# Performance work log

Measured on AMD Instinct MI355X. Metric: run time of the kernel, lower is better.

## Reference

```python
import jax, jax.numpy as jnp
import numpy as np

LAT = 512
FIN = 256
FOUT = 256
K = 3
N_STYLE = 4
B, H, W = 16, 64, 64


def setup_inputs() -> dict:
    key = jax.random.key(0)
    ks = jax.random.split(key, 8)
    x = jax.random.normal(ks[0], (B, FIN, H, W), dtype=jnp.float32)
    lat = jax.random.normal(ks[1], (B, LAT), dtype=jnp.float32)
    # main conv weight, kaiming_normal fan_in, leaky_relu a=0 -> gain sqrt(2)
    fan_in = FIN * K * K
    weight = jax.random.normal(ks[2], (FOUT, FIN, K, K), dtype=jnp.float32) * np.float32(np.sqrt(2.0 / fan_in))
    # EqualLinear layers: raw weight ~ N(0,1), runtime-scaled by 1/sqrt(in_dim)
    ws = jax.random.normal(ks[3], (N_STYLE, LAT, LAT), dtype=jnp.float32)
    bs = jnp.zeros((N_STYLE, LAT), dtype=jnp.float32)
    # final plain nn.Linear(lat_size, fin): uniform(-1/sqrt(in), 1/sqrt(in))
    bound = np.float32(1.0 / np.sqrt(LAT))
    wf = jax.random.uniform(ks[4], (FIN, LAT), dtype=jnp.float32, minval=-bound, maxval=bound)
    bf = jax.random.uniform(ks[5], (FIN,), dtype=jnp.float32, minval=-bound, maxval=bound)
    return {"x": x, "lat": lat, "weight": weight, "ws": ws, "bs": bs, "wf": wf, "bf": bf}


def reference(x, lat, weight, ws, bs, wf, bf):
    Bb, fin, Hh, Ww = x.shape
    fout, _, k, _ = weight.shape
    eq_scale = np.float32(1.0 / np.sqrt(lat.shape[1]))  # EqualLinear runtime scale

    # style MLP: n_layers_style x (EqualLinear + LeakyReLU(0.2)), then Linear -> fin
    h = lat
    for i in range(ws.shape[0]):
        h = jax.nn.leaky_relu(h @ (ws[i] * eq_scale).T + bs[i], 0.2)
    styles = h @ wf.T + bf  # [B, fin]

    # normalize base weight by inf-norm over (fin,k,k) per output channel
    wnorm = jnp.max(jnp.abs(weight), axis=(1, 2, 3), keepdims=True)
    mw = weight * (np.float32(1.0 / np.sqrt(fin * k * k)) / wnorm)  # [fout,fin,k,k]
    # normalize styles by inf-norm per sample
    styles = styles / jnp.max(jnp.abs(styles), axis=1, keepdims=True)

    # per-sample modulation + demodulation
    w = mw[None] * styles[:, None, :, None, None]  # [B,fout,fin,k,k]
    dcoefs = jax.lax.rsqrt(jnp.sum(w * w, axis=(2, 3, 4)) + 1e-8)  # [B,fout]
    w = w * dcoefs[:, :, None, None, None]
    w = w.reshape(Bb * fout, fin, k, k)

    # grouped conv with groups = batch (stride/dilation NOT passed in original -> 1)
    pad = (k - 1) // 2  # _get_same_padding with stride=1, dilation=1
    xg = x.reshape(1, Bb * fin, Hh, Ww)
    y = jax.lax.conv_general_dilated(
        xg, w, window_strides=(1, 1), padding=[(pad, pad), (pad, pad)],
        dimension_numbers=("NCHW", "OIHW", "NCHW"), feature_group_count=Bb)
    return y.reshape(Bb, fout, Hh, Ww)
```

## Files before the change

kernel.cpp:

```cpp
#include <hip/hip_runtime.h>
#include <hip/hip_bf16.h>

#define LATN 512
#define FINN 256
#define FOUTN 256
#define NB 16
#define HH 64
#define WW 64

typedef __attribute__((ext_vector_type(8))) short bf16x8;
typedef __attribute__((ext_vector_type(4))) float f32x4;
typedef __attribute__((ext_vector_type(4))) int i32x4;

#define WS_ZERO   0
#define WS_MW2    4096
#define WS_DCO    266240
#define WS_SNORM  282624
#define WS_WFMT   299008
#define WS_XM     1478656
#define WS_HA     (WS_XM)
#define WS_HB     (WS_XM + 32768)
#define WS_STY    (WS_XM + 65536)

__global__ void weight_prep_kernel(const float* __restrict__ weight,
                                   __hip_bfloat16* __restrict__ wfmt,
                                   float* __restrict__ mw2sum,
                                   float* __restrict__ zerobuf) {
    __shared__ float red[256];
    int o = blockIdx.x, t = threadIdx.x;
    if (o == 0 && t < 64) zerobuf[t] = 0.f;
    const float* wrow = weight + ((size_t)o * FINN + t) * 9;
    float wv[9];
    float mx = 0.f;
    #pragma unroll
    for (int k = 0; k < 9; ++k) { wv[k] = wrow[k]; mx = fmaxf(mx, fabsf(wv[k])); }
    red[t] = mx;
    __syncthreads();
    for (int k = 128; k > 0; k >>= 1) {
        if (t < k) red[t] = fmaxf(red[t], red[t + k]);
        __syncthreads();
    }
    float scale = (1.0f / 48.0f) / red[0];
    int obi = o >> 6, ol = o & 63, ch = t >> 5, il = t & 31;
    int slot = (il >> 3) ^ ((ol >> 1) & 3);
    char* basep = (char*)wfmt + (size_t)obi * 294912 + (size_t)ch * 36864
                + (size_t)ol * 64 + slot * 16 + (il & 7) * 2;
    float s2 = 0.f;
    #pragma unroll
    for (int tap = 0; tap < 9; ++tap) {
        float m = wv[tap] * scale;
        s2 += m * m;
        *(__hip_bfloat16*)(basep + tap * 4096) = __float2bfloat16(m);
    }
    mw2sum[(size_t)o * FINN + t] = s2;
}

__global__ __launch_bounds__(256) void style_layer_kernel(
    const float* __restrict__ in, const float* __restrict__ w,
    const float* __restrict__ bias, float* __restrict__ out,
    int in_dim_v4, int out_dim, float scale, int do_lrelu) {
    int t = threadIdx.x;
    int jl = t >> 4, kl = t & 15;
    int j = blockIdx.x * 16 + jl;
    int b = blockIdx.y;
    const float4* inr = (const float4*)(in + (size_t)b * (in_dim_v4 * 4));
    const float4* wr  = (const float4*)(w + (size_t)j * (in_dim_v4 * 4));
    float sum = 0.f;
    #pragma unroll 4
    for (int kb = kl; kb < in_dim_v4; kb += 16) {
        float4 wv = wr[kb], iv = inr[kb];
        sum += wv.x * iv.x + wv.y * iv.y + wv.z * iv.z + wv.w * iv.w;
    }
    #pragma unroll
    for (int off = 8; off >= 1; off >>= 1)
        sum += __shfl_xor(sum, off, 16);
    if (kl == 0) {
        float v = sum * scale + bias[j];
        if (do_lrelu && v < 0.f) v *= 0.2f;
        out[(size_t)b * out_dim + j] = v;
    }
}

__global__ __launch_bounds__(256) void norm_dcoef_kernel(
    const float* __restrict__ sty, const float* __restrict__ mw2,
    float* __restrict__ snorm, float* __restrict__ dco) {
    __shared__ float red[256];
    __shared__ float s2[256];
    int b = blockIdx.x, t = threadIdx.x;
    float v = sty[(size_t)b * FINN + t];
    red[t] = fabsf(v);
    __syncthreads();
    for (int k = 128; k > 0; k >>= 1) {
        if (t < k) red[t] = fmaxf(red[t], red[t + k]);
        __syncthreads();
    }
    float sv = v / red[0];
    snorm[(size_t)b * FINN + t] = sv;
    s2[t] = sv * sv;
    __syncthreads();
    const float4* m2 = (const float4*)(mw2 + (size_t)t * FINN);
    const float4* sq = (const float4*)s2;
    float sum = 0.f;
    #pragma unroll 8
    for (int kb = 0; kb < 64; ++kb) {
        float4 a = m2[kb], xq = sq[kb];
        sum += a.x * xq.x + a.y * xq.y + a.z * xq.z + a.w * xq.w;
    }
    dco[(size_t)b * FOUTN + t] = rsqrtf(sum + 1e-8f);
}

__global__ __launch_bounds__(256) void xcvt_kernel(const float* __restrict__ x,
                                                   const float* __restrict__ sn,
                                                   char* __restrict__ xm) {
    __shared__ float tile[64][65];
    int h = blockIdx.x, b = blockIdx.y;
    int t = threadIdx.x;
    int wl_ = t & 63, ig = t >> 6;
    char* xmb = xm + (size_t)b * 2097152;
    for (int icb = 0; icb < 4; ++icb) {
        if (icb) __syncthreads();
        #pragma unroll
        for (int p = 0; p < 16; ++p) {
            int i_l = p * 4 + ig;
            int i = icb * 64 + i_l;
            tile[i_l][wl_] = x[((size_t)(b * FINN + i)) * 4096 + h * 64 + wl_]
                             * sn[(size_t)b * FINN + i];
        }
        __syncthreads();
        #pragma unroll
        for (int rep = 0; rep < 2; ++rep) {
            int g = rep * 256 + t;
            int w = g >> 3, q8 = g & 7;
            int chunk = icb * 2 + (q8 >> 2), iq = q8 & 3;
            int slot = iq ^ (((h + 1) + ((w + 1) >> 1)) & 3);
            short tmp[8];
            #pragma unroll
            for (int j = 0; j < 8; ++j) {
                __hip_bfloat16 hb = __float2bfloat16(tile[q8 * 8 + j][w]);
                tmp[j] = *(short*)&hb;
            }
            char* dst = xmb + (size_t)chunk * 262144 + (size_t)(h * 64 + w) * 64 + slot * 16;
            *(bf16x8*)dst = *(bf16x8*)tmp;
        }
    }
}

__device__ __forceinline__ void gl_lds16(const void* g, void* l) {
    __builtin_amdgcn_global_load_lds(
        (const __attribute__((address_space(1))) unsigned int*)g,
        (__attribute__((address_space(3))) unsigned int*)l, 16, 0, 0);
}

__device__ __forceinline__ void rd_tap(bf16x8* xf, bf16x8* wf,
                                       const char* xsb, const char* wlb,
                                       int wid, int l15, int lg, int wfrag,
                                       int kh, int kw) {
    int tap = kh * 3 + kw;
    int pos0 = (wid + kh) * 66 + kw + l15;
    int xoff = pos0 * 64 + ((lg ^ ((pos0 >> 1) & 3)) << 4);
    #pragma unroll
    for (int nt = 0; nt < 4; ++nt)
        xf[nt] = *(const bf16x8*)(xsb + xoff + nt * 1024);
    #pragma unroll
    for (int mt = 0; mt < 4; ++mt)
        wf[mt] = *(const bf16x8*)(wlb + tap * 4096 + mt * 1024 + wfrag);
}

__device__ __forceinline__ void mm_tap(f32x4 acc[4][4], const bf16x8* xf, const bf16x8* wf) {
    #pragma unroll
    for (int mt = 0; mt < 4; ++mt)
        #pragma unroll
        for (int nt = 0; nt < 4; ++nt)
            acc[mt][nt] = __builtin_amdgcn_mfma_f32_16x16x32_bf16(
                wf[mt], xf[nt], acc[mt][nt], 0, 0, 0);
}

#define STEP(XFN, WFN, KH, KW, XFC, WFC)                                \
    rd_tap(XFN, WFN, xsb, wlb, wid, l15, lg, wfrag, KH, KW);            \
    __builtin_amdgcn_sched_barrier(0);                                  \
    asm volatile("s_waitcnt lgkmcnt(8)" ::: "memory");                  \
    __builtin_amdgcn_sched_barrier(0);                                  \
    __builtin_amdgcn_s_setprio(1);                                      \
    mm_tap(acc, XFC, WFC);                                              \
    __builtin_amdgcn_s_setprio(0);

__global__ __launch_bounds__(512, 2) void mconv_kernel(
    const char* __restrict__ xm, const char* __restrict__ wfmt,
    const float* __restrict__ dco, const float* __restrict__ zerobuf,
    float* __restrict__ y) {
    __shared__ char xs[2][42240];
    __shared__ char wl[2][36864];

    int t = threadIdx.x;
    int lane = t & 63;
    int wid = t >> 6;
    int h0 = blockIdx.x * 8;
    int obi = blockIdx.y;
    int b = blockIdx.z;

    if (t < 160) {
        int bufi = t / 80, u = t % 80;
        int r = u >> 3, sub = u & 7;
        int col = (sub >> 2) * 65, slot = sub & 3;
        *(i32x4*)(xs[bufi] + ((r * 66 + col) * 4 + slot) * 16) = (i32x4){0, 0, 0, 0};
    }

    const char* xmb = xm + (size_t)b * 2097152;
    const char* xsrc[5];
    unsigned xinc[5];
    unsigned xdst[5];
    #pragma unroll
    for (int q = 0; q < 5; ++q) {
        int idx = wid * 5 + q;
        int r = idx >> 2, quarter = idx & 3;
        int gh = h0 - 1 + r;
        bool v = (gh >= 0) && (gh < HH);
        xsrc[q] = v ? xmb + (size_t)(gh * 64 + quarter * 16) * 64 + lane * 16
                    : (const char*)zerobuf;
        xinc[q] = v ? 262144u : 0u;
        xdst[q] = (unsigned)((r * 66 + 1) * 64 + quarter * 1024);
    }
    const char* wlane = wfmt + (size_t)obi * 294912 + lane * 16;

    f32x4 acc[4][4] = {};
    int l15 = lane & 15, lg = lane >> 4;
    int wfrag = l15 * 64 + ((lg ^ ((l15 >> 1) & 3)) << 4);

    #pragma unroll
    for (int q = 0; q < 5; ++q) {
        gl_lds16(xsrc[q], xs[0] + xdst[q]);
        xsrc[q] += xinc[q];
    }
    #pragma unroll
    for (int q = 0; q < 5; ++q) {
        int idx = wid + q * 8;
        if (idx < 36) gl_lds16(wlane + idx * 1024, wl[0] + idx * 1024);
    }
    wlane += 36864;
    asm volatile("s_waitcnt vmcnt(0)" ::: "memory");
    __builtin_amdgcn_s_barrier();
    __builtin_amdgcn_sched_barrier(0);

    for (int ch = 0; ch < 8; ++ch) {
        int cur = ch & 1;
        if (ch < 7) {
            #pragma unroll
            for (int q = 0; q < 5; ++q) {
                gl_lds16(xsrc[q], xs[cur ^ 1] + xdst[q]);
                xsrc[q] += xinc[q];
            }
            #pragma unroll
            for (int q = 0; q < 5; ++q) {
                int idx = wid + q * 8;
                if (idx < 36) gl_lds16(wlane + idx * 1024, wl[cur ^ 1] + idx * 1024);
            }
            wlane += 36864;
        }
        const char* xsb = xs[cur];
        const char* wlb = wl[cur];

        bf16x8 xf0[4], wf0[4], xf1[4], wf1[4];
        rd_tap(xf0, wf0, xsb, wlb, wid, l15, lg, wfrag, 0, 0);
        STEP(xf1, wf1, 0, 1, xf0, wf0)
        STEP(xf0, wf0, 0, 2, xf1, wf1)
        STEP(xf1, wf1, 1, 0, xf0, wf0)
        STEP(xf0, wf0, 1, 1, xf1, wf1)
        STEP(xf1, wf1, 1, 2, xf0, wf0)
        STEP(xf0, wf0, 2, 0, xf1, wf1)
        STEP(xf1, wf1, 2, 1, xf0, wf0)
        STEP(xf0, wf0, 2, 2, xf1, wf1)
        __builtin_amdgcn_sched_barrier(0);
        asm volatile("s_waitcnt lgkmcnt(0)" ::: "memory");
        __builtin_amdgcn_sched_barrier(0);
        __builtin_amdgcn_s_setprio(1);
        mm_tap(acc, xf0, wf0);
        __builtin_amdgcn_s_setprio(0);

        asm volatile("s_waitcnt vmcnt(0)" ::: "memory");
        __builtin_amdgcn_s_barrier();
        __builtin_amdgcn_sched_barrier(0);
    }

    const float* dcb = dco + (size_t)b * FOUTN + obi * 64;
    float* yb = y + (((size_t)b * FOUTN + obi * 64) * HH + (h0 + wid)) * WW;
    #pragma unroll
    for (int mt = 0; mt < 4; ++mt) {
        #pragma unroll
        for (int j = 0; j < 4; ++j) {
            int o_l = mt * 16 + lg * 4 + j;
            float d = dcb[o_l];
            #pragma unroll
            for (int nt = 0; nt < 4; ++nt)
                yb[(size_t)o_l * 4096 + nt * 16 + l15] = acc[mt][nt][j] * d;
        }
    }
}

extern "C" void kernel_launch(void* const* d_in, const int* in_sizes, int n_in,
                              void* d_out, int out_size, void* d_ws, size_t ws_size,
                              hipStream_t stream) {
    const float* x      = (const float*)d_in[0];
    const float* lat    = (const float*)d_in[1];
    const float* weight = (const float*)d_in[2];
    const float* wsm    = (const float*)d_in[3];
    const float* bsm    = (const float*)d_in[4];
    const float* wff    = (const float*)d_in[5];
    const float* bff    = (const float*)d_in[6];
    float* y = (float*)d_out;

    char* base = (char*)d_ws;
    float* zerobuf = (float*)(base + WS_ZERO);
    float* mw2     = (float*)(base + WS_MW2);
    float* dco     = (float*)(base + WS_DCO);
    float* snorm   = (float*)(base + WS_SNORM);
    __hip_bfloat16* wfmt = (__hip_bfloat16*)(base + WS_WFMT);
    char* xm       = base + WS_XM;
    float* hA      = (float*)(base + WS_HA);
    float* hB      = (float*)(base + WS_HB);
    float* sty     = (float*)(base + WS_STY);

    const float eq = 0.044194173824159216f;

    weight_prep_kernel<<<FOUTN, 256, 0, stream>>>(weight, wfmt, mw2, zerobuf);
    style_layer_kernel<<<dim3(LATN / 16, NB), 256, 0, stream>>>(
        lat, wsm + 0 * (size_t)LATN * LATN, bsm + 0 * LATN, hA, LATN / 4, LATN, eq, 1);
    style_layer_kernel<<<dim3(LATN / 16, NB), 256, 0, stream>>>(
        hA, wsm + 1 * (size_t)LATN * LATN, bsm + 1 * LATN, hB, LATN / 4, LATN, eq, 1);
    style_layer_kernel<<<dim3(LATN / 16, NB), 256, 0, stream>>>(
        hB, wsm + 2 * (size_t)LATN * LATN, bsm + 2 * LATN, hA, LATN / 4, LATN, eq, 1);
    style_layer_kernel<<<dim3(LATN / 16, NB), 256, 0, stream>>>(
        hA, wsm + 3 * (size_t)LATN * LATN, bsm + 3 * LATN, hB, LATN / 4, LATN, eq, 1);
    style_layer_kernel<<<dim3(FINN / 16, NB), 256, 0, stream>>>(
        hB, wff, bff, sty, LATN / 4, FINN, 1.0f, 0);
    norm_dcoef_kernel<<<NB, 256, 0, stream>>>(sty, mw2, snorm, dco);
    xcvt_kernel<<<dim3(HH, NB), 256, 0, stream>>>(x, snorm, xm);
    mconv_kernel<<<dim3(8, 4, NB), 512, 0, stream>>>(xm, (const char*)wfmt, dco, zerobuf, y);
}
```

Baseline: 118.2 us.

## Double output rows per wave and single-buffer the activation tile in the modulated conv

Each wave now computes two output rows (16 per block) instead of one, so each weight fragment read from LDS feeds twice as many MFMAs and the grid is halved. The activation LDS tile is now a single larger buffer, loaded at the start of each channel chunk. Only the weights stay double-buffered, and out-of-range halo rows are zero-filled once instead of being read from a zero buffer. This raises register pressure (accumulators double, to 32 f32x4), puts the activation load latency on the critical path of every chunk, and halves the number of blocks, which may reduce occupancy.

```diff
diff --git a/kernel.cpp b/kernel.cpp
--- a/kernel.cpp
+++ b/kernel.cpp
@@ -151,147 +151,154 @@
         (__attribute__((address_space(3))) unsigned int*)l, 16, 0, 0);
 }
 
-__device__ __forceinline__ void rd_tap(bf16x8* xf, bf16x8* wf,
-                                       const char* xsb, const char* wlb,
-                                       int wid, int l15, int lg, int wfrag,
-                                       int kh, int kw) {
+__device__ __forceinline__ void rd_tap2(bf16x8* xf, bf16x8* wf,
+                                        const char* xsb, const char* wlb,
+                                        int wid, int l15, int lg, int wfrag,
+                                        int kh, int kw) {
     int tap = kh * 3 + kw;
-    int pos0 = (wid + kh) * 66 + kw + l15;
-    int xoff = pos0 * 64 + ((lg ^ ((pos0 >> 1) & 3)) << 4);
+    int pa = (wid * 2 + kh) * 66 + kw + l15;
+    int pb = pa + 66;
+    int xa = pa * 64 + ((lg ^ ((pa >> 1) & 3)) << 4);
+    int xb = pb * 64 + ((lg ^ ((pb >> 1) & 3)) << 4);
     #pragma unroll
     for (int nt = 0; nt < 4; ++nt)
-        xf[nt] = *(const bf16x8*)(xsb + xoff + nt * 1024);
+        xf[nt] = *(const bf16x8*)(xsb + xa + nt * 1024);
+    #pragma unroll
+    for (int nt = 0; nt < 4; ++nt)
+        xf[4 + nt] = *(const bf16x8*)(xsb + xb + nt * 1024);
     #pragma unroll
     for (int mt = 0; mt < 4; ++mt)
         wf[mt] = *(const bf16x8*)(wlb + tap * 4096 + mt * 1024 + wfrag);
 }
 
-__device__ __forceinline__ void mm_tap(f32x4 acc[4][4], const bf16x8* xf, const bf16x8* wf) {
+__device__ __forceinline__ void mm_tap2(f32x4 acc[4][8], const bf16x8* xf, const bf16x8* wf) {
     #pragma unroll
     for (int mt = 0; mt < 4; ++mt)
         #pragma unroll
-        for (int nt = 0; nt < 4; ++nt)
+        for (int nt = 0; nt < 8; ++nt)
             acc[mt][nt] = __builtin_amdgcn_mfma_f32_16x16x32_bf16(
                 wf[mt], xf[nt], acc[mt][nt], 0, 0, 0);
 }
 
-#define STEP(XFN, WFN, KH, KW, XFC, WFC)                                \
-    rd_tap(XFN, WFN, xsb, wlb, wid, l15, lg, wfrag, KH, KW);            \
+#define STEP2(XFN, WFN, KH, KW, XFC, WFC)                               \
+    rd_tap2(XFN, WFN, xs, wlb, wid, l15, lg, wfrag, KH, KW);            \
     __builtin_amdgcn_sched_barrier(0);                                  \
-    asm volatile("s_waitcnt lgkmcnt(8)" ::: "memory");                  \
+    asm volatile("s_waitcnt lgkmcnt(12)" ::: "memory");                 \
     __builtin_amdgcn_sched_barrier(0);                                  \
     __builtin_amdgcn_s_setprio(1);                                      \
-    mm_tap(acc, XFC, WFC);                                              \
+    mm_tap2(acc, XFC, WFC);                                             \
     __builtin_amdgcn_s_setprio(0);
 
 __global__ __launch_bounds__(512, 2) void mconv_kernel(
     const char* __restrict__ xm, const char* __restrict__ wfmt,
-    const float* __restrict__ dco, const float* __restrict__ zerobuf,
-    float* __restrict__ y) {
-    __shared__ char xs[2][42240];
+    const float* __restrict__ dco, float* __restrict__ y) {
+    __shared__ char xs[76032];
     __shared__ char wl[2][36864];
 
     int t = threadIdx.x;
     int lane = t & 63;
     int wid = t >> 6;
-    int h0 = blockIdx.x * 8;
+    int h0 = blockIdx.x * 16;
     int obi = blockIdx.y;
     int b = blockIdx.z;
 
-    if (t < 160) {
-        int bufi = t / 80, u = t % 80;
-        int r = u >> 3, sub = u & 7;
+    if (t < 144) {
+        int r = t >> 3, sub = t & 7;
         int col = (sub >> 2) * 65, slot = sub & 3;
-        *(i32x4*)(xs[bufi] + ((r * 66 + col) * 4 + slot) * 16) = (i32x4){0, 0, 0, 0};
-    }
-
-    const char* xmb = xm + (size_t)b * 2097152;
-    const char* xsrc[5];
-    unsigned xinc[5];
-    unsigned xdst[5];
-    #pragma unroll
-    for (int q = 0; q < 5; ++q) {
-        int idx = wid * 5 + q;
+        *(i32x4*)(xs + ((r * 66 + col) * 4 + slot) * 16) = (i32x4){0, 0, 0, 0};
+    }
+    if (h0 == 0) {
+        for (int e = t; e < 256; e += 512)
+            *(i32x4*)(xs + ((0 * 66 + 1 + (e >> 2)) * 4 + (e & 3)) * 16) = (i32x4){0, 0, 0, 0};
+    }
+    if (h0 == 48) {
+        for (int e = t; e < 256; e += 512)
+            *(i32x4*)(xs + ((17 * 66 + 1 + (e >> 2)) * 4 + (e & 3)) * 16) = (i32x4){0, 0, 0, 0};
+    }
+
+    const char* xmb = xm + (size_t)b * 2097152 + lane * 16;
+    unsigned xoff[9], xdst[9];
+    bool xval[9];
+    #pragma unroll
+    for (int q = 0; q < 9; ++q) {
+        int idx = wid * 9 + q;
         int r = idx >> 2, quarter = idx & 3;
         int gh = h0 - 1 + r;
-        bool v = (gh >= 0) && (gh < HH);
-        xsrc[q] = v ? xmb + (size_t)(gh * 64 + quarter * 16) * 64 + lane * 16
-                    : (const char*)zerobuf;
-        xinc[q] = v ? 262144u : 0u;
+        xval[q] = (gh >= 0) && (gh < HH);
+        xoff[q] = (unsigned)((gh * 64 + quarter * 16) * 64);
         xdst[q] = (unsigned)((r * 66 + 1) * 64 + quarter * 1024);
     }
     const char* wlane = wfmt + (size_t)obi * 294912 + lane * 16;
 
-    f32x4 acc[4][4] = {};
+    f32x4 acc[4][8] = {};
     int l15 = lane & 15, lg = lane >> 4;
     int wfrag = l15 * 64 + ((lg ^ ((l15 >> 1) & 3)) << 4);
 
-    #pragma unroll
-    for (int q = 0; q < 5; ++q) {
-        gl_lds16(xsrc[q], xs[0] + xdst[q]);
-        xsrc[q] += xinc[q];
-    }
     #pragma unroll
     for (int q = 0; q < 5; ++q) {
         int idx = wid + q * 8;
         if (idx < 36) gl_lds16(wlane + idx * 1024, wl[0] + idx * 1024);
     }
     wlane += 36864;
-    asm volatile("s_waitcnt vmcnt(0)" ::: "memory");
-    __builtin_amdgcn_s_barrier();
-    __builtin_amdgcn_sched_barrier(0);
 
     for (int ch = 0; ch < 8; ++ch) {
         int cur = ch & 1;
+        const char* xch = xmb + (size_t)ch * 262144;
+        #pragma unroll
+        for (int q = 0; q < 9; ++q)
+            if (xval[q]) gl_lds16(xch + xoff[q], xs + xdst[q]);
         if (ch < 7) {
-            #pragma unroll
-            for (int q = 0; q < 5; ++q) {
-                gl_lds16(xsrc[q], xs[cur ^ 1] + xdst[q]);
-                xsrc[q] += xinc[q];
-            }
             #pragma unroll
             for (int q = 0; q < 5; ++q) {
                 int idx = wid + q * 8;
                 if (idx < 36) gl_lds16(wlane + idx * 1024, wl[cur ^ 1] + idx * 1024);
             }
             wlane += 36864;
+            if (wid < 4) asm volatile("s_waitcnt vmcnt(5)" ::: "memory");
+            else         asm volatile("s_waitcnt vmcnt(4)" ::: "memory");
+        } else {
+            asm volatile("s_waitcnt vmcnt(0)" ::: "memory");
         }
-        const char* xsb = xs[cur];
+        asm volatile("s_waitcnt lgkmcnt(0)" ::: "memory");
+        __builtin_amdgcn_s_barrier();
+        __builtin_amdgcn_sched_barrier(0);
+
         const char* wlb = wl[cur];
-
-        bf16x8 xf0[4], wf0[4], xf1[4], wf1[4];
-        rd_tap(xf0, wf0, xsb, wlb, wid, l15, lg, wfrag, 0, 0);
-        STEP(xf1, wf1, 0, 1, xf0, wf0)
-        STEP(xf0, wf0, 0, 2, xf1, wf1)
-        STEP(xf1, wf1, 1, 0, xf0, wf0)
-        STEP(xf0, wf0, 1, 1, xf1, wf1)
-        STEP(xf1, wf1, 1, 2, xf0, wf0)
-        STEP(xf0, wf0, 2, 0, xf1, wf1)
-        STEP(xf1, wf1, 2, 1, xf0, wf0)
-        STEP(xf0, wf0, 2, 2, xf1, wf1)
+        bf16x8 xf0[8], wf0[4], xf1[8], wf1[4];
+        rd_tap2(xf0, wf0, xs, wlb, wid, l15, lg, wfrag, 0, 0);
+        STEP2(xf1, wf1, 0, 1, xf0, wf0)
+        STEP2(xf0, wf0, 0, 2, xf1, wf1)
+        STEP2(xf1, wf1, 1, 0, xf0, wf0)
+        STEP2(xf0, wf0, 1, 1, xf1, wf1)
+        STEP2(xf1, wf1, 1, 2, xf0, wf0)
+        STEP2(xf0, wf0, 2, 0, xf1, wf1)
+        STEP2(xf1, wf1, 2, 1, xf0, wf0)
+        STEP2(xf0, wf0, 2, 2, xf1, wf1)
         __builtin_amdgcn_sched_barrier(0);
         asm volatile("s_waitcnt lgkmcnt(0)" ::: "memory");
         __builtin_amdgcn_sched_barrier(0);
         __builtin_amdgcn_s_setprio(1);
-        mm_tap(acc, xf0, wf0);
+        mm_tap2(acc, xf0, wf0);
         __builtin_amdgcn_s_setprio(0);
 
-        asm volatile("s_waitcnt vmcnt(0)" ::: "memory");
         __builtin_amdgcn_s_barrier();
         __builtin_amdgcn_sched_barrier(0);
     }
 
     const float* dcb = dco + (size_t)b * FOUTN + obi * 64;
-    float* yb = y + (((size_t)b * FOUTN + obi * 64) * HH + (h0 + wid)) * WW;
-    #pragma unroll
-    for (int mt = 0; mt < 4; ++mt) {
-        #pragma unroll
-        for (int j = 0; j < 4; ++j) {
-            int o_l = mt * 16 + lg * 4 + j;
-            float d = dcb[o_l];
+    #pragma unroll
+    for (int rr = 0; rr < 2; ++rr) {
+        float* yb = y + (((size_t)b * FOUTN + obi * 64) * HH + (h0 + wid * 2 + rr)) * WW;
+        #pragma unroll
+        for (int mt = 0; mt < 4; ++mt) {
             #pragma unroll
-            for (int nt = 0; nt < 4; ++nt)
-                yb[(size_t)o_l * 4096 + nt * 16 + l15] = acc[mt][nt][j] * d;
+            for (int j = 0; j < 4; ++j) {
+                int o_l = mt * 16 + lg * 4 + j;
+                float d = dcb[o_l];
+                #pragma unroll
+                for (int n4 = 0; n4 < 4; ++n4)
+                    yb[(size_t)o_l * 4096 + n4 * 16 + l15] = acc[mt][rr * 4 + n4][j] * d;
+            }
         }
     }
 }
@@ -334,5 +341,5 @@
         hB, wff, bff, sty, LATN / 4, FINN, 1.0f, 0);
     norm_dcoef_kernel<<<NB, 256, 0, stream>>>(sty, mw2, snorm, dco);
     xcvt_kernel<<<dim3(HH, NB), 256, 0, stream>>>(x, snorm, xm);
-    mconv_kernel<<<dim3(8, 4, NB), 512, 0, stream>>>(xm, (const char*)wfmt, dco, zerobuf, y);
-}
+    mconv_kernel<<<dim3(4, 4, NB), 512, 0, stream>>>(xm, (const char*)wfmt, dco, y);
+}
```

Measured after the change: 148.4 us. 1.26x slower.
